# Kernel tuning notes

Measured on AMD Instinct MI355X. Metric: run time of the kernel, lower is better.

## Reference

```python
import jax, jax.numpy as jnp
import numpy as np
import math

N, T, D, H = 64, 512, 1024, 1024

def setup_inputs() -> dict:
    key = jax.random.key(0)
    k1, k2, k3, k4 = jax.random.split(key, 4)
    x = jax.random.normal(k1, (N, T, D), dtype=jnp.float32)
    h0 = jax.random.normal(k2, (N, H), dtype=jnp.float32)
    Wx = jax.random.normal(k3, (D, 4 * H), dtype=jnp.float32) / math.sqrt(D)
    Wh = jax.random.normal(k4, (H, 4 * H), dtype=jnp.float32) / math.sqrt(H)
    b = jnp.zeros((4 * H,), dtype=jnp.float32)
    return {"x": x, "h0": h0, "Wx": Wx, "Wh": Wh, "b": b}

def lstm_forward(x, h0, Wx, Wh, b):
    Hd = h0.shape[1]
    # Precompute input-to-hidden contribution for all timesteps in one GEMM.
    xW = jnp.einsum('ntd,dg->ntg', x, Wx) + b  # (N, T, 4H)
    c0 = jnp.zeros_like(h0)

    def step(carry, xw_t):
        prev_h, prev_c = carry
        a = xw_t + prev_h @ Wh  # (N, 4H)
        i = jax.nn.sigmoid(a[:, :Hd])
        f = jax.nn.sigmoid(a[:, Hd:2 * Hd])
        o = jax.nn.sigmoid(a[:, 2 * Hd:3 * Hd])
        g = jnp.tanh(a[:, 3 * Hd:])
        next_c = f * prev_c + i * g
        next_h = o * jnp.tanh(next_c)
        return (next_h, next_c), next_h

    # scan over time axis: move T to leading dim
    (_, _), hs = jax.lax.scan(step, (h0, c0), jnp.swapaxes(xW, 0, 1))
    return jnp.swapaxes(hs, 0, 1)  # (N, T, H)

def reference(x, h0, Wx, Wh, b):
    return lstm_forward(x, h0, Wx, Wh, b)
```

## Files before the change

### kernel.cpp

```cpp
#include <hip/hip_runtime.h>


#define NB 64
#define TT 512
#define DD 1024
#define HH 1024
#define GG 4096
#define FSTRIDE 32

using f32x4  = __attribute__((ext_vector_type(4))) float;
using bf16x8 = __attribute__((ext_vector_type(8))) __bf16;
using u16x4  = __attribute__((ext_vector_type(4))) unsigned short;

__device__ inline unsigned short f2bf(float x) {
  union { float f; unsigned u; } v; v.f = x;
  unsigned r = v.u + 0x7fffu + ((v.u >> 16) & 1u);
  return (unsigned short)(r >> 16);
}
__device__ inline float bfu2f(unsigned short u) {
  union { unsigned u; float f; } v; v.u = ((unsigned)u) << 16; return v.f;
}
__device__ inline float sigm(float x)     { return 1.0f / (1.0f + __expf(-x)); }
__device__ inline float tanhfast(float x) { return 1.0f - 2.0f / (__expf(2.0f * x) + 1.0f); }

__global__ __launch_bounds__(256) void tcast(const float* __restrict__ in,
                                             unsigned short* __restrict__ out,
                                             int rows, int cols) {
  __shared__ float tile[32][33];
  const int bx = blockIdx.x * 32;
  const int by = blockIdx.y * 32;
  const int tx = threadIdx.x;
  for (int i = threadIdx.y; i < 32; i += 8)
    tile[i][tx] = in[(size_t)(by + i) * cols + bx + tx];
  __syncthreads();
  for (int i = threadIdx.y; i < 32; i += 8)
    out[(size_t)(bx + i) * rows + by + tx] = f2bf(tile[tx][i]);
}

__global__ __launch_bounds__(256) void init_h(const float* __restrict__ h0,
                                              unsigned* __restrict__ hp0,
                                              unsigned* __restrict__ hp1,
                                              int* __restrict__ bar) {
  const int idx = blockIdx.x * 256 + threadIdx.x;
  const float v = h0[idx];
  const unsigned short hi = f2bf(v);
  const unsigned short lo = f2bf(v - bfu2f(hi));
  hp0[idx] = ((unsigned)hi << 16) | ((unsigned)(lo & 0xFFFEu));
  hp1[idx] = 1u;
  if (blockIdx.x == 0)
    for (int i = threadIdx.x; i < 256 * FSTRIDE; i += 256) bar[i] = 0;
}

#define BM 128
#define BN 128
#define BK 64
#define LDP (BK + 8)

__global__ __launch_bounds__(256) void gemm_xw(const float* __restrict__ x,
                                               const unsigned short* __restrict__ WxT,
                                               const float* __restrict__ bvec,
                                               unsigned short* __restrict__ xw) {
  __shared__ unsigned short As[BM][LDP];
  __shared__ unsigned short Bs[BN][LDP];
  const int tid  = threadIdx.x;
  const int m0   = blockIdx.y * BM;
  const int g0   = blockIdx.x * BN;
  const int wave = tid >> 6, lane = tid & 63;
  const int wm = (wave & 1) * 64, wn = (wave >> 1) * 64;
  const int lr = lane & 15, lk = (lane >> 4) * 8;

  f32x4 acc[4][4] = {};

  for (int kt = 0; kt < DD; kt += BK) {
#pragma unroll
    for (int it = 0; it < 8; ++it) {
      const int row = it * 16 + (tid >> 4);
      const int c4  = (tid & 15) * 4;
      const float4 xv = *(const float4*)(x + (size_t)(m0 + row) * DD + kt + c4);
      u16x4 us; us.x = f2bf(xv.x); us.y = f2bf(xv.y); us.z = f2bf(xv.z); us.w = f2bf(xv.w);
      *(u16x4*)&As[row][c4] = us;
    }
#pragma unroll
    for (int it = 0; it < 4; ++it) {
      const int row = it * 32 + (tid >> 3);
      const int c8  = (tid & 7) * 8;
      const uint4 wv = *(const uint4*)(WxT + (size_t)(g0 + row) * DD + kt + c8);
      *(uint4*)&Bs[row][c8] = wv;
    }
    __syncthreads();
#pragma unroll
    for (int ks = 0; ks < BK / 32; ++ks) {
      const int kk = ks * 32 + lk;
      bf16x8 af[4], bfv[4];
#pragma unroll
      for (int mi = 0; mi < 4; ++mi) af[mi]  = *(const bf16x8*)&As[wm + mi * 16 + lr][kk];
#pragma unroll
      for (int ni = 0; ni < 4; ++ni) bfv[ni] = *(const bf16x8*)&Bs[wn + ni * 16 + lr][kk];
#pragma unroll
      for (int mi = 0; mi < 4; ++mi)
#pragma unroll
        for (int ni = 0; ni < 4; ++ni)
          acc[mi][ni] = __builtin_amdgcn_mfma_f32_16x16x32_bf16(af[mi], bfv[ni], acc[mi][ni], 0, 0, 0);
    }
    __syncthreads();
  }

#pragma unroll
  for (int mi = 0; mi < 4; ++mi) {
    const int row = m0 + wm + mi * 16 + ((lane >> 4) << 2);
#pragma unroll
    for (int ni = 0; ni < 4; ++ni) {
      const int col = g0 + wn + ni * 16 + lr;
      const float bb = bvec[col];
#pragma unroll
      for (int j = 0; j < 4; ++j)
        xw[(size_t)(row + j) * GG + col] = f2bf(acc[mi][ni][j] + bb);
    }
  }
}

__global__ __launch_bounds__(512, 1) void lstm_seq(
    const unsigned short* __restrict__ WhT,
    const unsigned short* __restrict__ xw,
    unsigned* __restrict__ hp0, unsigned* __restrict__ hp1,
    float* __restrict__ out, int* __restrict__ bar) {
  __shared__ unsigned short As_hi[16][1024];
  __shared__ unsigned short As_lo[16][1024];
  __shared__ float abuf[4][16][34];

  const int tid  = threadIdx.x;
  const int bid  = blockIdx.x;
  const int grp  = bid & 3;
  const int qid  = bid >> 2;
  const int r0   = grp * 16;
  const int j0   = qid * 32;
  const int w    = tid >> 6;
  const int gate = w & 3;
  const int ch   = w >> 2;
  const int lane = tid & 63;
  const int lr   = lane & 15;
  const int kslot = lane >> 4;
  const int sx   = lr & 7;
  const int srow = tid >> 5;
  const int swr  = srow & 7;
  const int re   = tid >> 5, ce = tid & 31;

  int* myflag = &bar[(grp * 32 + qid) * FSTRIDE];

  bf16x8 rB[32];
  {
    const unsigned short* wrow =
        WhT + ((size_t)(gate * HH + j0 + ch * 16 + lr)) * HH + kslot * 8;
#pragma unroll
    for (int ks = 0; ks < 32; ++ks)
      rB[ks] = *(const bf16x8*)&wrow[ks * 32];
  }

  float creg = 0.0f;

  const size_t xrc = (size_t)(r0 + re) * TT * GG + j0 + ce;
  unsigned short xc0 = xw[xrc + 0 * HH];
  unsigned short xc1 = xw[xrc + 1 * HH];
  unsigned short xc2 = xw[xrc + 2 * HH];
  unsigned short xc3 = xw[xrc + 3 * HH];

  for (int t = 0; t < TT; ++t) {
    unsigned* hp = (t & 1) ? hp1 : hp0;
    unsigned* np = (t & 1) ? hp0 : hp1;

    if (t > 0 && tid < 32) {
      const int* fp = &bar[(grp * 32 + tid) * FSTRIDE];
      int v = __hip_atomic_load(fp, __ATOMIC_RELAXED, __HIP_MEMORY_SCOPE_AGENT);
      while (v < t) {
        __builtin_amdgcn_s_sleep(2);
        v = __hip_atomic_load(fp, __ATOMIC_RELAXED, __HIP_MEMORY_SCOPE_AGENT);
      }
    }
    __syncthreads();

    const unsigned* hrow = hp + (size_t)(r0 + srow) * HH;
    const int c0 = 0 * 32 + (tid & 31), c1 = 1 * 32 + (tid & 31);
    const int c2 = 2 * 32 + (tid & 31), c3 = 3 * 32 + (tid & 31);
    const unsigned* p0 = hrow + c0 * 8;
    const unsigned* p1 = hrow + c1 * 8;
    const unsigned* p2 = hrow + c2 * 8;
    const unsigned* p3 = hrow + c3 * 8;
    const unsigned expect = (unsigned)((t >> 1) & 1);
    uint4 q0, q1, q2, q3, q4, q5, q6, q7;
    for (int rtry = 0;; ++rtry) {
      asm volatile(
          "global_load_dwordx4 %0, %[a0], off sc0 sc1\n\t"
          "global_load_dwordx4 %1, %[a0], off offset:16 sc0 sc1\n\t"
          "global_load_dwordx4 %2, %[a1], off sc0 sc1\n\t"
          "global_load_dwordx4 %3, %[a1], off offset:16 sc0 sc1\n\t"
          "global_load_dwordx4 %4, %[a2], off sc0 sc1\n\t"
          "global_load_dwordx4 %5, %[a2], off offset:16 sc0 sc1\n\t"
          "global_load_dwordx4 %6, %[a3], off sc0 sc1\n\t"
          "global_load_dwordx4 %7, %[a3], off offset:16 sc0 sc1\n\t"
          "s_waitcnt vmcnt(0)"
          : "=&v"(q0), "=&v"(q1), "=&v"(q2), "=&v"(q3),
            "=&v"(q4), "=&v"(q5), "=&v"(q6), "=&v"(q7)
          : [a0] "v"(p0), [a1] "v"(p1), [a2] "v"(p2), [a3] "v"(p3)
          : "memory");
      const unsigned av = q0.x & q0.y & q0.z & q0.w & q1.x & q1.y & q1.z & q1.w &
                          q2.x & q2.y & q2.z & q2.w & q3.x & q3.y & q3.z & q3.w &
                          q4.x & q4.y & q4.z & q4.w & q5.x & q5.y & q5.z & q5.w &
                          q6.x & q6.y & q6.z & q6.w & q7.x & q7.y & q7.z & q7.w;
      const unsigned ov = q0.x | q0.y | q0.z | q0.w | q1.x | q1.y | q1.z | q1.w |
                          q2.x | q2.y | q2.z | q2.w | q3.x | q3.y | q3.z | q3.w |
                          q4.x | q4.y | q4.z | q4.w | q5.x | q5.y | q5.z | q5.w |
                          q6.x | q6.y | q6.z | q6.w | q7.x | q7.y | q7.z | q7.w;
      const unsigned chk = expect ? av : ~ov;
      if (chk & 1u) break;
      __builtin_amdgcn_s_sleep(1);
    }

#define UNPACK(QA, QB, CC)                                                    \
    {                                                                         \
      const int sc = (CC) ^ swr;                                              \
      uint4 HI, LO;                                                           \
      HI.x = (QA.x >> 16) | (QA.y & 0xffff0000u);                             \
      HI.y = (QA.z >> 16) | (QA.w & 0xffff0000u);                             \
      HI.z = (QB.x >> 16) | (QB.y & 0xffff0000u);                             \
      HI.w = (QB.z >> 16) | (QB.w & 0xffff0000u);                             \
      LO.x = (QA.x & 0xffffu) | (QA.y << 16);                                 \
      LO.y = (QA.z & 0xffffu) | (QA.w << 16);                                 \
      LO.z = (QB.x & 0xffffu) | (QB.y << 16);                                 \
      LO.w = (QB.z & 0xffffu) | (QB.w << 16);                                 \
      *(uint4*)&As_hi[srow][sc * 8] = HI;                                     \
      *(uint4*)&As_lo[srow][sc * 8] = LO;                                     \
    }
    UNPACK(q0, q1, c0) UNPACK(q2, q3, c1) UNPACK(q4, q5, c2) UNPACK(q6, q7, c3)
#undef UNPACK
    __syncthreads();

    const int tn = (t + 1 < TT) ? t + 1 : t;
    const size_t xa = xrc + (size_t)tn * GG;
    const unsigned short nx0 = xw[xa + 0 * HH];
    const unsigned short nx1 = xw[xa + 1 * HH];
    const unsigned short nx2 = xw[xa + 2 * HH];
    const unsigned short nx3 = xw[xa + 3 * HH];

    f32x4 aHE = {}, aHO = {}, aLE = {}, aLO = {};
#pragma unroll
    for (int ks = 0; ks < 32; ks += 2) {
      const int cc0 = ((ks)     * 4 + kslot) ^ sx;
      const int cc1 = ((ks + 1) * 4 + kslot) ^ sx;
      const bf16x8 ah0 = *(const bf16x8*)&As_hi[lr][cc0 * 8];
      const bf16x8 al0 = *(const bf16x8*)&As_lo[lr][cc0 * 8];
      const bf16x8 ah1 = *(const bf16x8*)&As_hi[lr][cc1 * 8];
      const bf16x8 al1 = *(const bf16x8*)&As_lo[lr][cc1 * 8];
      aHE = __builtin_amdgcn_mfma_f32_16x16x32_bf16(ah0, rB[ks],     aHE, 0, 0, 0);
      aLE = __builtin_amdgcn_mfma_f32_16x16x32_bf16(al0, rB[ks],     aLE, 0, 0, 0);
      aHO = __builtin_amdgcn_mfma_f32_16x16x32_bf16(ah1, rB[ks + 1], aHO, 0, 0, 0);
      aLO = __builtin_amdgcn_mfma_f32_16x16x32_bf16(al1, rB[ks + 1], aLO, 0, 0, 0);
    }
    const f32x4 accv = (aHE + aHO) + (aLE + aLO);

#pragma unroll
    for (int j = 0; j < 4; ++j)
      abuf[gate][(lane >> 4) * 4 + j][ch * 16 + lr] = accv[j];
    __syncthreads();

    const float ai = abuf[0][re][ce] + bfu2f(xc0);
    const float af = abuf[1][re][ce] + bfu2f(xc1);
    const float ao = abuf[2][re][ce] + bfu2f(xc2);
    const float ag = abuf[3][re][ce] + bfu2f(xc3);

    const float gi = sigm(ai), gf = sigm(af), go = sigm(ao), gg = tanhfast(ag);
    creg = gf * creg + gi * gg;
    const float hn = go * tanhfast(creg);

    out[((size_t)(r0 + re) * TT + t) * HH + j0 + ce] = hn;
    const unsigned short hi = f2bf(hn);
    const unsigned short lo = f2bf(hn - bfu2f(hi));
    const unsigned tag = (unsigned)(((t + 1) >> 1) & 1);
    const unsigned pack = ((unsigned)hi << 16) | ((unsigned)(lo & 0xFFFEu) | tag);
    __hip_atomic_store(&np[(size_t)(r0 + re) * HH + j0 + ce], pack,
                       __ATOMIC_RELAXED, __HIP_MEMORY_SCOPE_AGENT);

    xc0 = nx0; xc1 = nx1; xc2 = nx2; xc3 = nx3;

    if (t + 1 < TT) {
      __syncthreads();
      if (tid == 0)
        __hip_atomic_store(myflag, t + 1, __ATOMIC_RELAXED, __HIP_MEMORY_SCOPE_AGENT);
    }
  }
}

extern "C" void kernel_launch(void* const* d_in, const int* in_sizes, int n_in,
                              void* d_out, int out_size, void* d_ws, size_t ws_size,
                              hipStream_t stream) {
  const float* x  = (const float*)d_in[0];
  const float* h0 = (const float*)d_in[1];
  const float* Wx = (const float*)d_in[2];
  const float* Wh = (const float*)d_in[3];
  const float* b  = (const float*)d_in[4];
  float* out = (float*)d_out;

  unsigned short* xw  = (unsigned short*)d_ws;
  unsigned short* WxT = xw  + (size_t)NB * TT * GG;
  unsigned short* WhT = WxT + (size_t)GG * DD;
  unsigned* hp0 = (unsigned*)(WhT + (size_t)GG * HH);
  unsigned* hp1 = hp0 + (size_t)NB * HH;
  int* bar = (int*)(hp1 + (size_t)NB * HH);

  tcast<<<dim3(GG / 32, DD / 32), dim3(32, 8), 0, stream>>>(Wx, WxT, DD, GG);
  tcast<<<dim3(GG / 32, HH / 32), dim3(32, 8), 0, stream>>>(Wh, WhT, HH, GG);
  init_h<<<NB * HH / 256, 256, 0, stream>>>(h0, hp0, hp1, bar);
  gemm_xw<<<dim3(GG / BN, NB * TT / BM), 256, 0, stream>>>(x, WxT, b, xw);

  lstm_seq<<<128, 512, 0, stream>>>(WhT, xw, hp0, hp1, out, bar);
}
```

Baseline: 3.244 ms.

## Pre-cast x to bf16 and use direct global-to-LDS loads in input GEMM

Adds a separate kernel that converts x to bf16 in workspace, then a new input-projection GEMM that loads bf16 tiles straight into shared memory with global_load_lds and runs bf16 MFMA. This removes the fp32 load and in-kernel conversion from the GEMM's inner loop and halves the bytes it reads for x. The cost is an extra pass over x plus extra workspace. It falls back to the old GEMM if the workspace is too small. The GEMM is only part of a runtime dominated by the sequential recurrence.

```diff
diff --git a/kernel.cpp b/kernel.cpp
--- a/kernel.cpp
+++ b/kernel.cpp
@@ -22,6 +22,13 @@
 }
 __device__ inline float sigm(float x)     { return 1.0f / (1.0f + __expf(-x)); }
 __device__ inline float tanhfast(float x) { return 1.0f - 2.0f / (__expf(2.0f * x) + 1.0f); }
+
+typedef unsigned int u32t;
+__device__ inline void gl2lds16(const void* g, void* l) {
+  __builtin_amdgcn_global_load_lds(
+      (const __attribute__((address_space(1))) u32t*)g,
+      (__attribute__((address_space(3))) u32t*)l, 16, 0, 0);
+}
 
 __global__ __launch_bounds__(256) void tcast(const float* __restrict__ in,
                                              unsigned short* __restrict__ out,
@@ -37,6 +44,18 @@
     out[(size_t)(bx + i) * rows + by + tx] = f2bf(tile[tx][i]);
 }
 
+__global__ __launch_bounds__(256) void cast_x(const float* __restrict__ in,
+                                              unsigned short* __restrict__ outp) {
+  const size_t i = ((size_t)blockIdx.x * 256 + threadIdx.x) * 8;
+  const float4 a = *(const float4*)(in + i);
+  const float4 b = *(const float4*)(in + i + 4);
+  u16x4 ua, ub;
+  ua.x = f2bf(a.x); ua.y = f2bf(a.y); ua.z = f2bf(a.z); ua.w = f2bf(a.w);
+  ub.x = f2bf(b.x); ub.y = f2bf(b.y); ub.z = f2bf(b.z); ub.w = f2bf(b.w);
+  *(u16x4*)(outp + i)     = ua;
+  *(u16x4*)(outp + i + 4) = ub;
+}
+
 __global__ __launch_bounds__(256) void init_h(const float* __restrict__ h0,
                                               unsigned* __restrict__ hp0,
                                               unsigned* __restrict__ hp1,
@@ -49,6 +68,62 @@
   hp1[idx] = 1u;
   if (blockIdx.x == 0)
     for (int i = threadIdx.x; i < 256 * FSTRIDE; i += 256) bar[i] = 0;
+}
+
+__global__ __launch_bounds__(256) void gemm_xw2(const unsigned short* __restrict__ xb,
+                                                const unsigned short* __restrict__ WxT,
+                                                const float* __restrict__ bvec,
+                                                unsigned short* __restrict__ xw) {
+  __shared__ unsigned short As[128][64];
+  __shared__ unsigned short Bs[128][64];
+  const int tid  = threadIdx.x;
+  const int g0   = blockIdx.x * 128;
+  const int m0   = blockIdx.y * 128;
+  const int wave = tid >> 6, lane = tid & 63;
+  const int wm = (wave & 1) * 64, wn = (wave >> 1) * 64;
+  const int lr = lane & 15, lk = (lane >> 4) * 8;
+
+  f32x4 acc[4][4] = {};
+
+  for (int kt = 0; kt < DD; kt += 64) {
+#pragma unroll
+    for (int it = 0; it < 4; ++it) {
+      const int u   = it * 256 + tid;
+      const int row = u >> 3;
+      const int k8  = (u & 7) * 8;
+      gl2lds16(xb  + (size_t)(m0 + row) * DD + kt + k8, &As[0][0] + (size_t)u * 8);
+      gl2lds16(WxT + (size_t)(g0 + row) * DD + kt + k8, &Bs[0][0] + (size_t)u * 8);
+    }
+    __syncthreads();
+#pragma unroll
+    for (int ks = 0; ks < 2; ++ks) {
+      const int kk = ks * 32 + lk;
+      bf16x8 af[4], bfv[4];
+#pragma unroll
+      for (int mi = 0; mi < 4; ++mi) af[mi]  = *(const bf16x8*)&As[wm + mi * 16 + lr][kk];
+#pragma unroll
+      for (int ni = 0; ni < 4; ++ni) bfv[ni] = *(const bf16x8*)&Bs[wn + ni * 16 + lr][kk];
+#pragma unroll
+      for (int mi = 0; mi < 4; ++mi)
+#pragma unroll
+        for (int ni = 0; ni < 4; ++ni)
+          acc[mi][ni] = __builtin_amdgcn_mfma_f32_16x16x32_bf16(af[mi], bfv[ni], acc[mi][ni], 0, 0, 0);
+    }
+    __syncthreads();
+  }
+
+#pragma unroll
+  for (int mi = 0; mi < 4; ++mi) {
+    const int row = m0 + wm + mi * 16 + ((lane >> 4) << 2);
+#pragma unroll
+    for (int ni = 0; ni < 4; ++ni) {
+      const int col = g0 + wn + ni * 16 + lr;
+      const float bb = bvec[col];
+#pragma unroll
+      for (int j = 0; j < 4; ++j)
+        xw[(size_t)(row + j) * GG + col] = f2bf(acc[mi][ni][j] + bb);
+    }
+  }
 }
 
 #define BM 128
@@ -299,17 +374,33 @@
   const float* b  = (const float*)d_in[4];
   float* out = (float*)d_out;
 
+  const size_t xw_elems  = (size_t)NB * TT * GG;
+  const size_t xb_elems  = (size_t)NB * TT * DD;
+  const size_t wT_elems  = (size_t)GG * DD;
+  const size_t NH        = (size_t)NB * HH;
+
+  const size_t need = (xw_elems + xb_elems + 2 * wT_elems) * 2 +
+                      2 * NH * 4 + 256 * FSTRIDE * 4;
+  const bool use_xb = (ws_size >= need);
+
   unsigned short* xw  = (unsigned short*)d_ws;
-  unsigned short* WxT = xw  + (size_t)NB * TT * GG;
-  unsigned short* WhT = WxT + (size_t)GG * DD;
-  unsigned* hp0 = (unsigned*)(WhT + (size_t)GG * HH);
-  unsigned* hp1 = hp0 + (size_t)NB * HH;
-  int* bar = (int*)(hp1 + (size_t)NB * HH);
+  unsigned short* xb  = xw + xw_elems;
+  unsigned short* WxT = use_xb ? (xb + xb_elems) : (xw + xw_elems);
+  unsigned short* WhT = WxT + wT_elems;
+  unsigned* hp0 = (unsigned*)(WhT + wT_elems);
+  unsigned* hp1 = hp0 + NH;
+  int* bar = (int*)(hp1 + NH);
 
   tcast<<<dim3(GG / 32, DD / 32), dim3(32, 8), 0, stream>>>(Wx, WxT, DD, GG);
   tcast<<<dim3(GG / 32, HH / 32), dim3(32, 8), 0, stream>>>(Wh, WhT, HH, GG);
   init_h<<<NB * HH / 256, 256, 0, stream>>>(h0, hp0, hp1, bar);
-  gemm_xw<<<dim3(GG / BN, NB * TT / BM), 256, 0, stream>>>(x, WxT, b, xw);
+
+  if (use_xb) {
+    cast_x<<<(int)(xb_elems / (256 * 8)), 256, 0, stream>>>(x, xb);
+    gemm_xw2<<<dim3(GG / 128, NB * TT / 128), 256, 0, stream>>>(xb, WxT, b, xw);
+  } else {
+    gemm_xw<<<dim3(GG / BN, NB * TT / BM), 256, 0, stream>>>(x, WxT, b, xw);
+  }
 
   lstm_seq<<<128, 512, 0, stream>>>(WhT, xw, hp0, hp1, out, bar);
 }
```

Result: no change. 3.184 ms (-1.9%).

## Fuse input GEMM into recurrent kernel with producer blocks and chunk flags

Applied to the files above, without the earlier changes.

Merges the separate xW GEMM kernel into the persistent LSTM kernel. Blocks 128–255 compute xW chunks in time-major order and bump per-chunk counters. Blocks 0–127 run the recurrence and wait on each chunk counter before reading that step's xW. This overlaps the large input projection with the latency-bound sequential scan, at the cost of a second wait on every step. It also relies on all 256 blocks being resident at once to avoid deadlock.

```diff
diff --git a/kernel.cpp b/kernel.cpp
--- a/kernel.cpp
+++ b/kernel.cpp
@@ -7,6 +7,8 @@
 #define HH 1024
 #define GG 4096
 #define FSTRIDE 32
+#define NCHUNK 256
+#define CSTRIDE 8
 
 using f32x4  = __attribute__((ext_vector_type(4))) float;
 using bf16x8 = __attribute__((ext_vector_type(8))) __bf16;
@@ -48,88 +50,101 @@
   hp0[idx] = ((unsigned)hi << 16) | ((unsigned)(lo & 0xFFFEu));
   hp1[idx] = 1u;
   if (blockIdx.x == 0)
-    for (int i = threadIdx.x; i < 256 * FSTRIDE; i += 256) bar[i] = 0;
-}
-
-#define BM 128
-#define BN 128
-#define BK 64
-#define LDP (BK + 8)
-
-__global__ __launch_bounds__(256) void gemm_xw(const float* __restrict__ x,
-                                               const unsigned short* __restrict__ WxT,
-                                               const float* __restrict__ bvec,
-                                               unsigned short* __restrict__ xw) {
-  __shared__ unsigned short As[BM][LDP];
-  __shared__ unsigned short Bs[BN][LDP];
-  const int tid  = threadIdx.x;
-  const int m0   = blockIdx.y * BM;
-  const int g0   = blockIdx.x * BN;
-  const int wave = tid >> 6, lane = tid & 63;
-  const int wm = (wave & 1) * 64, wn = (wave >> 1) * 64;
-  const int lr = lane & 15, lk = (lane >> 4) * 8;
-
-  f32x4 acc[4][4] = {};
-
-  for (int kt = 0; kt < DD; kt += BK) {
-#pragma unroll
-    for (int it = 0; it < 8; ++it) {
-      const int row = it * 16 + (tid >> 4);
-      const int c4  = (tid & 15) * 4;
-      const float4 xv = *(const float4*)(x + (size_t)(m0 + row) * DD + kt + c4);
-      u16x4 us; us.x = f2bf(xv.x); us.y = f2bf(xv.y); us.z = f2bf(xv.z); us.w = f2bf(xv.w);
-      *(u16x4*)&As[row][c4] = us;
-    }
-#pragma unroll
-    for (int it = 0; it < 4; ++it) {
-      const int row = it * 32 + (tid >> 3);
-      const int c8  = (tid & 7) * 8;
-      const uint4 wv = *(const uint4*)(WxT + (size_t)(g0 + row) * DD + kt + c8);
-      *(uint4*)&Bs[row][c8] = wv;
-    }
-    __syncthreads();
-#pragma unroll
-    for (int ks = 0; ks < BK / 32; ++ks) {
-      const int kk = ks * 32 + lk;
-      bf16x8 af[4], bfv[4];
-#pragma unroll
-      for (int mi = 0; mi < 4; ++mi) af[mi]  = *(const bf16x8*)&As[wm + mi * 16 + lr][kk];
-#pragma unroll
-      for (int ni = 0; ni < 4; ++ni) bfv[ni] = *(const bf16x8*)&Bs[wn + ni * 16 + lr][kk];
-#pragma unroll
-      for (int mi = 0; mi < 4; ++mi)
-#pragma unroll
-        for (int ni = 0; ni < 4; ++ni)
-          acc[mi][ni] = __builtin_amdgcn_mfma_f32_16x16x32_bf16(af[mi], bfv[ni], acc[mi][ni], 0, 0, 0);
-    }
-    __syncthreads();
-  }
-
-#pragma unroll
-  for (int mi = 0; mi < 4; ++mi) {
-    const int row = m0 + wm + mi * 16 + ((lane >> 4) << 2);
-#pragma unroll
-    for (int ni = 0; ni < 4; ++ni) {
-      const int col = g0 + wn + ni * 16 + lr;
-      const float bb = bvec[col];
-#pragma unroll
-      for (int j = 0; j < 4; ++j)
-        xw[(size_t)(row + j) * GG + col] = f2bf(acc[mi][ni][j] + bb);
-    }
-  }
-}
-
-__global__ __launch_bounds__(512, 1) void lstm_seq(
+    for (int i = threadIdx.x; i < 256 * FSTRIDE + NCHUNK * CSTRIDE; i += 256)
+      bar[i] = 0;
+}
+
+__global__ __launch_bounds__(512, 1) void lstm_fused(
+    const float* __restrict__ x,
+    const unsigned short* __restrict__ WxT,
     const unsigned short* __restrict__ WhT,
-    const unsigned short* __restrict__ xw,
+    const float* __restrict__ bvec,
+    unsigned short* __restrict__ xw,
     unsigned* __restrict__ hp0, unsigned* __restrict__ hp1,
     float* __restrict__ out, int* __restrict__ bar) {
-  __shared__ unsigned short As_hi[16][1024];
-  __shared__ unsigned short As_lo[16][1024];
-  __shared__ float abuf[4][16][34];
-
-  const int tid  = threadIdx.x;
-  const int bid  = blockIdx.x;
+  __shared__ __align__(16) unsigned char smem[74240];
+  const int tid = threadIdx.x;
+  const int bid = blockIdx.x;
+  int* cnt = bar + 256 * FSTRIDE;
+
+  if (bid >= 128) {
+    unsigned short (*As)[72] = (unsigned short(*)[72])smem;
+    unsigned short (*Bs)[72] = (unsigned short(*)[72])(smem + 18432);
+    const int gid  = bid - 128;
+    const int wave = tid >> 6, lane = tid & 63;
+    const int wm = (wave & 1) * 64, wn = (wave >> 1) * 32;
+    const int lr = lane & 15, lk = (lane >> 4) * 8;
+
+    for (int tau = gid; tau < NCHUNK * 32; tau += 128) {
+      const int c  = tau >> 5;
+      const int n  = tau & 31;
+      const int m0 = c * 128;
+      const int g0 = n * 128;
+      f32x4 acc[4][2] = {};
+
+      for (int kt = 0; kt < DD; kt += 64) {
+#pragma unroll
+        for (int it = 0; it < 4; ++it) {
+          const int rl = it * 32 + (tid >> 4);
+          const int c4 = (tid & 15) * 4;
+          const int m  = m0 + rl;
+          const size_t xrow = (size_t)(m & 63) * TT + (m >> 6);
+          const float4 xv = *(const float4*)(x + xrow * DD + kt + c4);
+          u16x4 us; us.x = f2bf(xv.x); us.y = f2bf(xv.y);
+          us.z = f2bf(xv.z); us.w = f2bf(xv.w);
+          *(u16x4*)&As[rl][c4] = us;
+        }
+#pragma unroll
+        for (int it = 0; it < 2; ++it) {
+          const int rl = it * 64 + (tid >> 3);
+          const int c8 = (tid & 7) * 8;
+          const uint4 wv = *(const uint4*)(WxT + (size_t)(g0 + rl) * DD + kt + c8);
+          *(uint4*)&Bs[rl][c8] = wv;
+        }
+        __syncthreads();
+#pragma unroll
+        for (int ks = 0; ks < 2; ++ks) {
+          const int kk = ks * 32 + lk;
+          bf16x8 af[4], bfv[2];
+#pragma unroll
+          for (int mi = 0; mi < 4; ++mi) af[mi]  = *(const bf16x8*)&As[wm + mi * 16 + lr][kk];
+#pragma unroll
+          for (int ni = 0; ni < 2; ++ni) bfv[ni] = *(const bf16x8*)&Bs[wn + ni * 16 + lr][kk];
+#pragma unroll
+          for (int mi = 0; mi < 4; ++mi)
+#pragma unroll
+            for (int ni = 0; ni < 2; ++ni)
+              acc[mi][ni] = __builtin_amdgcn_mfma_f32_16x16x32_bf16(af[mi], bfv[ni], acc[mi][ni], 0, 0, 0);
+        }
+        __syncthreads();
+      }
+
+#pragma unroll
+      for (int mi = 0; mi < 4; ++mi) {
+        const int row = m0 + wm + mi * 16 + ((lane >> 4) << 2);
+#pragma unroll
+        for (int ni = 0; ni < 2; ++ni) {
+          const int col = g0 + wn + ni * 16 + lr;
+          const float bb = bvec[col];
+#pragma unroll
+          for (int j = 0; j < 4; ++j)
+            xw[(size_t)(row + j) * GG + col] = f2bf(acc[mi][ni][j] + bb);
+        }
+      }
+      __syncthreads();
+      if (tid == 0) {
+        __builtin_amdgcn_fence(__ATOMIC_RELEASE, "agent");
+        __hip_atomic_fetch_add(&cnt[c * CSTRIDE], 1,
+                               __ATOMIC_RELAXED, __HIP_MEMORY_SCOPE_AGENT);
+      }
+    }
+    return;
+  }
+
+  unsigned short (*As_hi)[1024] = (unsigned short(*)[1024])smem;
+  unsigned short (*As_lo)[1024] = (unsigned short(*)[1024])(smem + 32768);
+  float (*abuf)[16][34] = (float(*)[16][34])(smem + 65536);
+
   const int grp  = bid & 3;
   const int qid  = bid >> 2;
   const int r0   = grp * 16;
@@ -158,11 +173,19 @@
 
   float creg = 0.0f;
 
-  const size_t xrc = (size_t)(r0 + re) * TT * GG + j0 + ce;
-  unsigned short xc0 = xw[xrc + 0 * HH];
-  unsigned short xc1 = xw[xrc + 1 * HH];
-  unsigned short xc2 = xw[xrc + 2 * HH];
-  unsigned short xc3 = xw[xrc + 3 * HH];
+  const size_t xrowc = (size_t)(r0 + re) * GG + j0 + ce;
+#define XWADDR(u, g) ((size_t)(u) * ((size_t)NB * GG) + xrowc + (size_t)(g) * HH)
+
+  int last_c = 0;
+  if (tid == 32) {
+    while (__hip_atomic_load(&cnt[0], __ATOMIC_RELAXED, __HIP_MEMORY_SCOPE_AGENT) < 32)
+      __builtin_amdgcn_s_sleep(2);
+  }
+  __syncthreads();
+  unsigned short xc0 = xw[XWADDR(0, 0)];
+  unsigned short xc1 = xw[XWADDR(0, 1)];
+  unsigned short xc2 = xw[XWADDR(0, 2)];
+  unsigned short xc3 = xw[XWADDR(0, 3)];
 
   for (int t = 0; t < TT; ++t) {
     unsigned* hp = (t & 1) ? hp1 : hp0;
@@ -174,6 +197,16 @@
       while (v < t) {
         __builtin_amdgcn_s_sleep(2);
         v = __hip_atomic_load(fp, __ATOMIC_RELAXED, __HIP_MEMORY_SCOPE_AGENT);
+      }
+    }
+    if (tid == 32) {
+      const int u = (t + 1 < TT) ? (t + 1) : (TT - 1);
+      const int cn = u >> 1;
+      if (cn > last_c) {
+        while (__hip_atomic_load(&cnt[cn * CSTRIDE],
+                                 __ATOMIC_RELAXED, __HIP_MEMORY_SCOPE_AGENT) < 32)
+          __builtin_amdgcn_s_sleep(2);
+        last_c = cn;
       }
     }
     __syncthreads();
@@ -187,7 +220,7 @@
     const unsigned* p3 = hrow + c3 * 8;
     const unsigned expect = (unsigned)((t >> 1) & 1);
     uint4 q0, q1, q2, q3, q4, q5, q6, q7;
-    for (int rtry = 0;; ++rtry) {
+    for (;;) {
       asm volatile(
           "global_load_dwordx4 %0, %[a0], off sc0 sc1\n\t"
           "global_load_dwordx4 %1, %[a0], off offset:16 sc0 sc1\n\t"
@@ -235,11 +268,10 @@
     __syncthreads();
 
     const int tn = (t + 1 < TT) ? t + 1 : t;
-    const size_t xa = xrc + (size_t)tn * GG;
-    const unsigned short nx0 = xw[xa + 0 * HH];
-    const unsigned short nx1 = xw[xa + 1 * HH];
-    const unsigned short nx2 = xw[xa + 2 * HH];
-    const unsigned short nx3 = xw[xa + 3 * HH];
+    const unsigned short nx0 = xw[XWADDR(tn, 0)];
+    const unsigned short nx1 = xw[XWADDR(tn, 1)];
+    const unsigned short nx2 = xw[XWADDR(tn, 2)];
+    const unsigned short nx3 = xw[XWADDR(tn, 3)];
 
     f32x4 aHE = {}, aHO = {}, aLE = {}, aLO = {};
 #pragma unroll
@@ -287,6 +319,7 @@
         __hip_atomic_store(myflag, t + 1, __ATOMIC_RELAXED, __HIP_MEMORY_SCOPE_AGENT);
     }
   }
+#undef XWADDR
 }
 
 extern "C" void kernel_launch(void* const* d_in, const int* in_sizes, int n_in,
@@ -299,17 +332,20 @@
   const float* b  = (const float*)d_in[4];
   float* out = (float*)d_out;
 
+  const size_t xw_elems = (size_t)NB * TT * GG;
+  const size_t wT_elems = (size_t)GG * DD;
+  const size_t NH       = (size_t)NB * HH;
+
   unsigned short* xw  = (unsigned short*)d_ws;
-  unsigned short* WxT = xw  + (size_t)NB * TT * GG;
-  unsigned short* WhT = WxT + (size_t)GG * DD;
-  unsigned* hp0 = (unsigned*)(WhT + (size_t)GG * HH);
-  unsigned* hp1 = hp0 + (size_t)NB * HH;
-  int* bar = (int*)(hp1 + (size_t)NB * HH);
+  unsigned short* WxT = xw + xw_elems;
+  unsigned short* WhT = WxT + wT_elems;
+  unsigned* hp0 = (unsigned*)(WhT + wT_elems);
+  unsigned* hp1 = hp0 + NH;
+  int* bar = (int*)(hp1 + NH);
 
   tcast<<<dim3(GG / 32, DD / 32), dim3(32, 8), 0, stream>>>(Wx, WxT, DD, GG);
   tcast<<<dim3(GG / 32, HH / 32), dim3(32, 8), 0, stream>>>(Wh, WhT, HH, GG);
   init_h<<<NB * HH / 256, 256, 0, stream>>>(h0, hp0, hp1, bar);
-  gemm_xw<<<dim3(GG / BN, NB * TT / BM), 256, 0, stream>>>(x, WxT, b, xw);
-
-  lstm_seq<<<128, 512, 0, stream>>>(WhT, xw, hp0, hp1, out, bar);
-}
+
+  lstm_fused<<<256, 512, 0, stream>>>(x, WxT, WhT, b, xw, hp0, hp1, out, bar);
+}
```

New measurement: 2.681 ms. -17.3%, faster.
